# Kernel optimization log

Hardware: AMD Instinct MI355X
Metric: run time of the kernel (lower is better)

Reference implementation:

```python
import jax, jax.numpy as jnp
import numpy as np

B, NPG, KMAX, DIN, DOUT = 64, 2048, 64, 256, 256
HEADS, HDIM, EDIM = 2, 8, 16


def _ln(x, g, b, eps=1e-5):
    m = x.mean(-1, keepdims=True)
    v = x.var(-1, keepdims=True)
    return (x - m) / jnp.sqrt(v + eps) * g + b


def _lin_init(key, fan_in, fan_out):
    # xavier_uniform with gain=0.5 as in _init_weights
    lim = 0.5 * np.sqrt(6.0 / (fan_in + fan_out))
    return jax.random.uniform(key, (fan_in, fan_out), jnp.float32, -lim, lim)


def setup_inputs() -> dict:
    key = jax.random.key(0)
    ks = jax.random.split(key, 16)
    N = B * NPG
    inp = {
        "x": jax.random.normal(ks[0], (N, DIN), jnp.float32),
        # roughly orthonormal-scale eigenvector columns
        "eigenvectors": jax.random.normal(ks[1], (N, KMAX), jnp.float32) / np.sqrt(NPG),
        "eigenvalues": jax.random.uniform(ks[2], (B * KMAX,), jnp.float32, 0.0, 2.0),
        "eig_mask": jnp.ones((B * KMAX,), bool),
        "batch": jnp.repeat(jnp.arange(B, dtype=jnp.int32), NPG),
        "bsz": B,
        # eig_encoder: Linear(1,16), LayerNorm(16), ReLU, Linear(16,16)
        "W1": _lin_init(ks[3], 1, EDIM), "b1": jnp.zeros(EDIM),
        "g1": jnp.ones(EDIM), "be1": jnp.zeros(EDIM),
        "W2": _lin_init(ks[4], EDIM, EDIM), "b2": jnp.zeros(EDIM),
        # MultiheadAttention(16, 2 heads)
        "Wq": _lin_init(ks[5], EDIM, EDIM), "bq": jnp.zeros(EDIM),
        "Wk": _lin_init(ks[6], EDIM, EDIM), "bk": jnp.zeros(EDIM),
        "Wv": _lin_init(ks[7], EDIM, EDIM), "bv": jnp.zeros(EDIM),
        "Wo": _lin_init(ks[8], EDIM, EDIM), "bo": jnp.zeros(EDIM),
        # filter_generator: Linear(16,32), ReLU, Linear(32,1), Tanh
        "Wf1": _lin_init(ks[9], EDIM, 32), "bf1": jnp.zeros(32),
        "Wf2": _lin_init(ks[10], 32, 1), "bf2": jnp.zeros(1),
        # output_proj: Linear(in_dim,out_dim), LayerNorm(out_dim)
        "Wp": _lin_init(ks[11], DIN, DOUT), "bp": jnp.zeros(DOUT),
        "gp": jnp.ones(DOUT), "bep": jnp.zeros(DOUT),
    }
    return inp


def reference(x, eigenvectors, eigenvalues, eig_mask, batch, bsz,
              W1, b1, g1, be1, W2, b2,
              Wq, bq, Wk, bk, Wv, bv, Wo, bo,
              Wf1, bf1, Wf2, bf2, Wp, bp, gp, bep):
    N, D = x.shape
    k_max = eigenvalues.shape[0] // bsz
    ev = eigenvalues.reshape(bsz, k_max)            # [B, k]
    m = eig_mask.reshape(bsz, k_max)                # [B, k] valid mask

    # eig_encoder
    h = jnp.maximum(_ln(ev[..., None] @ W1 + b1, g1, be1), 0.0) @ W2 + b2  # [B, k, 16]

    # multi-head self-attention over eigenvalue tokens (eval mode, no dropout)
    q = (h @ Wq + bq).reshape(bsz, k_max, HEADS, HDIM)
    kk = (h @ Wk + bk).reshape(bsz, k_max, HEADS, HDIM)
    v = (h @ Wv + bv).reshape(bsz, k_max, HEADS, HDIM)
    scores = jnp.einsum('bqhd,bkhd->bhqk', q, kk) / np.sqrt(HDIM)
    scores = jnp.where(m[:, None, None, :], scores, -1e9)  # key_padding_mask
    attn = jax.nn.softmax(scores, axis=-1)
    ctx = jnp.einsum('bhqk,bkhd->bqhd', attn, v).reshape(bsz, k_max, EDIM)
    ctx = ctx @ Wo + bo

    # per-eigenvalue scalar filters, zeroed at padded slots
    filt = jnp.tanh(jnp.maximum(ctx @ Wf1 + bf1, 0.0) @ Wf2 + bf2)[..., 0]  # [B, k]
    filt = filt * m

    # batched spectral filtering (equal-size graphs: N = bsz * npg)
    npg = N // bsz
    xg = x.reshape(bsz, npg, D)
    vg = eigenvectors.reshape(bsz, npg, k_max)
    x_freq = jnp.einsum('bnk,bnd->bkd', vg, xg)                # U^T x
    x_spatial = jnp.einsum('bnk,bkd->bnd', vg, filt[..., None] * x_freq)  # U diag(f) U^T x

    # output_proj: Linear + LayerNorm
    return _ln(x_spatial.reshape(N, D) @ Wp + bp, gp, bep)
```

## Files before the change

kernel.cpp:

```cpp
#include <hip/hip_runtime.h>
#include <math.h>

#define BATCH 64
#define NPG   2048
#define KMAX  64
#define DIN   256
#define DOUT  256
#define S_SPLIT 8

typedef __attribute__((ext_vector_type(4))) float f32x4;
typedef __attribute__((ext_vector_type(8))) short bf16x8;

__device__ __forceinline__ unsigned short f2b(float f) {
    unsigned int u = __float_as_uint(f);
    u = (u + 0x7fffu + ((u >> 16) & 1u)) >> 16;
    return (unsigned short)u;
}
__device__ __forceinline__ float b2f(unsigned short h) {
    return __uint_as_float(((unsigned int)h) << 16);
}
__device__ __forceinline__ unsigned int pk2(float a, float b) {
    return (unsigned int)f2b(a) | ((unsigned int)f2b(b) << 16);
}

__global__ __launch_bounds__(64) void k_filt(
    const float* __restrict__ ev,
    const float* __restrict__ W1, const float* __restrict__ b1,
    const float* __restrict__ g1, const float* __restrict__ be1,
    const float* __restrict__ W2, const float* __restrict__ b2,
    const float* __restrict__ Wq, const float* __restrict__ bq,
    const float* __restrict__ Wk, const float* __restrict__ bk,
    const float* __restrict__ Wv, const float* __restrict__ bv,
    const float* __restrict__ Wo, const float* __restrict__ bo,
    const float* __restrict__ Wf1, const float* __restrict__ bf1,
    const float* __restrict__ Wf2, const float* __restrict__ bf2,
    float* __restrict__ filt)
{
    int b = blockIdx.x;
    int t = threadIdx.x;
    __shared__ float kk_l[64][16];
    __shared__ float v_l[64][16];

    float e = ev[b * KMAX + t];

    float h0[16];
    float mean = 0.f;
    #pragma unroll
    for (int j = 0; j < 16; j++) { h0[j] = e * W1[j] + b1[j]; mean += h0[j]; }
    mean *= (1.f / 16.f);
    float var = 0.f;
    #pragma unroll
    for (int j = 0; j < 16; j++) { float d = h0[j] - mean; var += d * d; }
    var *= (1.f / 16.f);
    float rstd = rsqrtf(var + 1e-5f);
    #pragma unroll
    for (int j = 0; j < 16; j++)
        h0[j] = fmaxf((h0[j] - mean) * rstd * g1[j] + be1[j], 0.f);

    float h[16];
    #pragma unroll
    for (int j = 0; j < 16; j++) {
        float a = b2[j];
        #pragma unroll
        for (int i = 0; i < 16; i++) a += h0[i] * W2[i * 16 + j];
        h[j] = a;
    }

    float q[16];
    #pragma unroll
    for (int j = 0; j < 16; j++) {
        float aq = bq[j], ak = bk[j], av = bv[j];
        #pragma unroll
        for (int i = 0; i < 16; i++) {
            float hi = h[i];
            aq += hi * Wq[i * 16 + j];
            ak += hi * Wk[i * 16 + j];
            av += hi * Wv[i * 16 + j];
        }
        q[j] = aq; kk_l[t][j] = ak; v_l[t][j] = av;
    }
    __syncthreads();

    float ctx[16];
    const float scale = 0.35355339059327373f;
    #pragma unroll
    for (int hd = 0; hd < 2; hd++) {
        float mx = -1e30f;
        for (int u = 0; u < 64; u++) {
            float s = 0.f;
            #pragma unroll
            for (int d = 0; d < 8; d++) s += q[hd * 8 + d] * kk_l[u][hd * 8 + d];
            mx = fmaxf(mx, s * scale);
        }
        float den = 0.f;
        float c[8] = {0, 0, 0, 0, 0, 0, 0, 0};
        for (int u = 0; u < 64; u++) {
            float s = 0.f;
            #pragma unroll
            for (int d = 0; d < 8; d++) s += q[hd * 8 + d] * kk_l[u][hd * 8 + d];
            float p = expf(s * scale - mx);
            den += p;
            #pragma unroll
            for (int d = 0; d < 8; d++) c[d] += p * v_l[u][hd * 8 + d];
        }
        float r = 1.f / den;
        #pragma unroll
        for (int d = 0; d < 8; d++) ctx[hd * 8 + d] = c[d] * r;
    }

    float c2[16];
    #pragma unroll
    for (int j = 0; j < 16; j++) {
        float a = bo[j];
        #pragma unroll
        for (int i = 0; i < 16; i++) a += ctx[i] * Wo[i * 16 + j];
        c2[j] = a;
    }

    float acc = bf2[0];
    #pragma unroll
    for (int j = 0; j < 32; j++) {
        float a = bf1[j];
        #pragma unroll
        for (int i = 0; i < 16; i++) a += c2[i] * Wf1[i * 32 + j];
        acc += fmaxf(a, 0.f) * Wf2[j];
    }
    filt[b * KMAX + t] = tanhf(acc);
}

__global__ __launch_bounds__(256) void k_xfreq(
    const float* __restrict__ x,
    const float* __restrict__ evec,
    unsigned short* __restrict__ part)
{
    int b = blockIdx.x;
    int s = blockIdx.y;
    int tid = threadIdx.x;
    int kg = tid >> 5;
    int dg = tid & 31;
    const int NS = NPG / S_SPLIT;
    int n0 = s * NS;

    __shared__ float xl[16][DIN];
    __shared__ float vl[16][KMAX];

    float acc[8][8];
    #pragma unroll
    for (int i = 0; i < 8; i++)
        #pragma unroll
        for (int j = 0; j < 8; j++) acc[i][j] = 0.f;

    for (int c = 0; c < NS; c += 16) {
        const float4* xsrc = (const float4*)(x + (size_t)(b * NPG + n0 + c) * DIN);
        const float4* vsrc = (const float4*)(evec + (size_t)(b * NPG + n0 + c) * KMAX);
        #pragma unroll
        for (int r = 0; r < 4; r++)
            ((float4*)xl)[r * 256 + tid] = xsrc[r * 256 + tid];
        ((float4*)vl)[tid] = vsrc[tid];
        __syncthreads();

        #pragma unroll 4
        for (int i = 0; i < 16; i++) {
            float4 va = *(const float4*)&vl[i][kg * 8];
            float4 vb = *(const float4*)&vl[i][kg * 8 + 4];
            float vk[8] = {va.x, va.y, va.z, va.w, vb.x, vb.y, vb.z, vb.w};
            float xd[8];
            #pragma unroll
            for (int j = 0; j < 8; j++) xd[j] = xl[i][dg + j * 32];
            #pragma unroll
            for (int kk = 0; kk < 8; kk++)
                #pragma unroll
                for (int j = 0; j < 8; j++)
                    acc[kk][j] += vk[kk] * xd[j];
        }
        __syncthreads();
    }

    unsigned short* dst = part + ((size_t)s * BATCH + b) * KMAX * DIN;
    #pragma unroll
    for (int kk = 0; kk < 8; kk++) {
        int k = kg * 8 + kk;
        #pragma unroll
        for (int j = 0; j < 8; j++)
            dst[k * DIN + dg + j * 32] = f2b(acc[kk][j]);
    }
}

__global__ __launch_bounds__(256) void k_gspec(
    const unsigned short* __restrict__ part, const float* __restrict__ filt,
    const float* __restrict__ Wp, unsigned short* __restrict__ g_frag)
{
    int b = blockIdx.x;
    int sg = blockIdx.y;
    int s = sg >> 2, g = sg & 3;
    int d = threadIdx.x;

    __shared__ float fxl[8][257];

    #pragma unroll
    for (int j = 0; j < 8; j++) {
        int k = 32 * s + 8 * g + j;
        float a = 0.f;
        #pragma unroll
        for (int ss = 0; ss < S_SPLIT; ss++)
            a += b2f(part[((size_t)(ss * BATCH + b) * KMAX + k) * DIN + d]);
        fxl[j][d] = a * filt[b * KMAX + k];
    }
    __syncthreads();

    float a[8] = {0.f, 0.f, 0.f, 0.f, 0.f, 0.f, 0.f, 0.f};
    #pragma unroll 4
    for (int dd = 0; dd < 256; dd++) {
        float w = Wp[(size_t)dd * DOUT + d];
        #pragma unroll
        for (int j = 0; j < 8; j++) a[j] += fxl[j][dd] * w;
    }

    int t = d >> 4, c = d & 15;
    uint4 p;
    p.x = pk2(a[0], a[1]); p.y = pk2(a[2], a[3]);
    p.z = pk2(a[4], a[5]); p.w = pk2(a[6], a[7]);
    *(uint4*)&g_frag[(((size_t)(b * 2 + s) * 16 + t) * 64 + (g * 16 + c)) * 8] = p;
}

#define VG_P 72

__global__ __launch_bounds__(256) void k_out(
    const float* __restrict__ evec,
    const unsigned short* __restrict__ g_frag,
    const float* __restrict__ bp, const float* __restrict__ gp,
    const float* __restrict__ bep,
    float* __restrict__ out)
{
    int blk = blockIdx.x;
    int b = blk >> 5;
    int n0 = blk * 64;
    int tid = threadIdx.x;
    int w = tid >> 6;
    int lane = tid & 63;
    int c = lane & 15, g = lane >> 4;

    __shared__ unsigned short lds_vg[64 * VG_P];

    {
        const float4* src = (const float4*)(evec + (size_t)n0 * KMAX);
        #pragma unroll
        for (int r = 0; r < 4; r++) {
            int f = r * 256 + tid;
            float4 v = src[f];
            int n = f >> 4, kq = f & 15;
            uint2 p; p.x = pk2(v.x, v.y); p.y = pk2(v.z, v.w);
            *(uint2*)&lds_vg[n * VG_P + kq * 4] = p;
        }
    }
    __syncthreads();

    f32x4 acc[16];
    #pragma unroll
    for (int t = 0; t < 16; t++) acc[t] = (f32x4){0.f, 0.f, 0.f, 0.f};

    bf16x8 a0 = *(const bf16x8*)&lds_vg[(16 * w + c) * VG_P + 8 * g];
    bf16x8 a1 = *(const bf16x8*)&lds_vg[(16 * w + c) * VG_P + 32 + 8 * g];

    const bf16x8* gf = (const bf16x8*)(g_frag + (size_t)b * 2 * 16 * 64 * 8);
    #pragma unroll
    for (int t = 0; t < 16; t++) {
        bf16x8 bb = gf[t * 64 + lane];
        acc[t] = __builtin_amdgcn_mfma_f32_16x16x32_bf16(a0, bb, acc[t], 0, 0, 0);
    }
    #pragma unroll
    for (int t = 0; t < 16; t++) {
        bf16x8 bb = gf[(16 + t) * 64 + lane];
        acc[t] = __builtin_amdgcn_mfma_f32_16x16x32_bf16(a1, bb, acc[t], 0, 0, 0);
    }

    #pragma unroll
    for (int r = 0; r < 4; r++) {
        float s1 = 0.f, s2 = 0.f;
        #pragma unroll
        for (int t = 0; t < 16; t++) {
            float a = acc[t][r] + bp[16 * t + c];
            s1 += a; s2 += a * a;
        }
        #pragma unroll
        for (int off = 1; off < 16; off <<= 1) {
            s1 += __shfl_xor(s1, off, 64);
            s2 += __shfl_xor(s2, off, 64);
        }
        float mean = s1 * (1.f / DOUT);
        float rstd = rsqrtf(s2 * (1.f / DOUT) - mean * mean + 1e-5f);
        int row = n0 + 16 * w + 4 * g + r;
        #pragma unroll
        for (int t = 0; t < 16; t++) {
            float a = acc[t][r] + bp[16 * t + c];
            out[(size_t)row * DOUT + 16 * t + c] =
                (a - mean) * rstd * gp[16 * t + c] + bep[16 * t + c];
        }
    }
}

extern "C" void kernel_launch(void* const* d_in, const int* in_sizes, int n_in,
                              void* d_out, int out_size, void* d_ws, size_t ws_size,
                              hipStream_t stream) {
    const float* x    = (const float*)d_in[0];
    const float* evec = (const float*)d_in[1];
    const float* ev   = (const float*)d_in[2];
    const float* W1  = (const float*)d_in[6];
    const float* b1  = (const float*)d_in[7];
    const float* g1  = (const float*)d_in[8];
    const float* be1 = (const float*)d_in[9];
    const float* W2  = (const float*)d_in[10];
    const float* b2  = (const float*)d_in[11];
    const float* Wq  = (const float*)d_in[12];
    const float* bq  = (const float*)d_in[13];
    const float* Wk  = (const float*)d_in[14];
    const float* bk  = (const float*)d_in[15];
    const float* Wv  = (const float*)d_in[16];
    const float* bv  = (const float*)d_in[17];
    const float* Wo  = (const float*)d_in[18];
    const float* bo  = (const float*)d_in[19];
    const float* Wf1 = (const float*)d_in[20];
    const float* bf1 = (const float*)d_in[21];
    const float* Wf2 = (const float*)d_in[22];
    const float* bf2 = (const float*)d_in[23];
    const float* Wp  = (const float*)d_in[24];
    const float* bp  = (const float*)d_in[25];
    const float* gp  = (const float*)d_in[26];
    const float* bep = (const float*)d_in[27];

    unsigned short* part   = (unsigned short*)d_ws;
    unsigned short* g_frag = part + (size_t)S_SPLIT * BATCH * KMAX * DIN;
    float*          filt   = (float*)(g_frag + (size_t)BATCH * KMAX * DIN);
    float* out = (float*)d_out;

    k_filt<<<BATCH, 64, 0, stream>>>(ev, W1, b1, g1, be1, W2, b2,
                                     Wq, bq, Wk, bk, Wv, bv, Wo, bo,
                                     Wf1, bf1, Wf2, bf2, filt);
    k_xfreq<<<dim3(BATCH, S_SPLIT), 256, 0, stream>>>(x, evec, part);
    k_gspec<<<dim3(BATCH, 8), 256, 0, stream>>>(part, filt, Wp, g_frag);
    k_out<<<(BATCH * NPG) / 64, 256, 0, stream>>>(evec, g_frag,
                                                  bp, gp, bep, out);
}
```

Measured before the change: 490.1 us.

## Compute U^T x projection with bf16 MFMA instead of FP32 FMA loops

Rewrites the k_xfreq kernel so x and eigenvector tiles are loaded, converted to bf16, and packed into MFMA fragment layout in shared memory, then accumulated with 16x16x32 bf16 matrix-core instructions. The block grows to 512 threads, 8 waves, each owning a 16-row k tile and half of the d columns. This targets the scalar FMA cost of the old register-tiled loop, which likely dominated the biggest stage. It gives up input precision to bf16, and the global loads are strided, with each lane reading eight rows of one column.

Measured after the change: 464.5 us. 1.06x faster.

```diff
diff --git a/kernel.cpp b/kernel.cpp
--- a/kernel.cpp
+++ b/kernel.cpp
@@ -128,7 +128,7 @@
     filt[b * KMAX + t] = tanhf(acc);
 }
 
-__global__ __launch_bounds__(256) void k_xfreq(
+__global__ __launch_bounds__(512) void k_xfreq(
     const float* __restrict__ x,
     const float* __restrict__ evec,
     unsigned short* __restrict__ part)
@@ -136,53 +136,73 @@
     int b = blockIdx.x;
     int s = blockIdx.y;
     int tid = threadIdx.x;
-    int kg = tid >> 5;
-    int dg = tid & 31;
+    int w = tid >> 6;
+    int lane = tid & 63;
+    int c = lane & 15, g = lane >> 4;
     const int NS = NPG / S_SPLIT;
-    int n0 = s * NS;
-
-    __shared__ float xl[16][DIN];
-    __shared__ float vl[16][KMAX];
-
-    float acc[8][8];
-    #pragma unroll
-    for (int i = 0; i < 8; i++)
-        #pragma unroll
-        for (int j = 0; j < 8; j++) acc[i][j] = 0.f;
-
-    for (int c = 0; c < NS; c += 16) {
-        const float4* xsrc = (const float4*)(x + (size_t)(b * NPG + n0 + c) * DIN);
-        const float4* vsrc = (const float4*)(evec + (size_t)(b * NPG + n0 + c) * KMAX);
-        #pragma unroll
-        for (int r = 0; r < 4; r++)
-            ((float4*)xl)[r * 256 + tid] = xsrc[r * 256 + tid];
-        ((float4*)vl)[tid] = vsrc[tid];
+    int n0 = b * NPG + s * NS;
+
+    __shared__ unsigned short xB[2 * 16 * 64 * 8];
+    __shared__ unsigned short evA[2 * 4 * 64 * 8];
+
+    f32x4 acc[8];
+    #pragma unroll
+    for (int t = 0; t < 8; t++) acc[t] = (f32x4){0.f, 0.f, 0.f, 0.f};
+
+    int mt = w & 3;
+    int dh = w >> 2;
+
+    for (int ch = 0; ch < NS; ch += 64) {
+        #pragma unroll
+        for (int i = 0; i < 4; i++) {
+            int idx = w * 4 + i;
+            int s2 = idx >> 4, t = idx & 15;
+            const float* src = x + (size_t)(n0 + ch + 32 * s2 + 8 * g) * DIN
+                                 + 16 * t + c;
+            float v[8];
+            #pragma unroll
+            for (int j = 0; j < 8; j++) v[j] = src[(size_t)j * DIN];
+            uint4 p;
+            p.x = pk2(v[0], v[1]); p.y = pk2(v[2], v[3]);
+            p.z = pk2(v[4], v[5]); p.w = pk2(v[6], v[7]);
+            *(uint4*)&xB[((size_t)idx * 64 + lane) * 8] = p;
+        }
+        {
+            int s2 = w >> 2, kt = w & 3;
+            const float* src = evec + (size_t)(n0 + ch + 32 * s2 + 8 * g) * KMAX
+                                    + 16 * kt + c;
+            float v[8];
+            #pragma unroll
+            for (int j = 0; j < 8; j++) v[j] = src[(size_t)j * KMAX];
+            uint4 p;
+            p.x = pk2(v[0], v[1]); p.y = pk2(v[2], v[3]);
+            p.z = pk2(v[4], v[5]); p.w = pk2(v[6], v[7]);
+            *(uint4*)&evA[((size_t)w * 64 + lane) * 8] = p;
+        }
         __syncthreads();
 
-        #pragma unroll 4
-        for (int i = 0; i < 16; i++) {
-            float4 va = *(const float4*)&vl[i][kg * 8];
-            float4 vb = *(const float4*)&vl[i][kg * 8 + 4];
-            float vk[8] = {va.x, va.y, va.z, va.w, vb.x, vb.y, vb.z, vb.w};
-            float xd[8];
-            #pragma unroll
-            for (int j = 0; j < 8; j++) xd[j] = xl[i][dg + j * 32];
-            #pragma unroll
-            for (int kk = 0; kk < 8; kk++)
-                #pragma unroll
-                for (int j = 0; j < 8; j++)
-                    acc[kk][j] += vk[kk] * xd[j];
+        #pragma unroll
+        for (int s2 = 0; s2 < 2; s2++) {
+            bf16x8 a = *(const bf16x8*)&evA[((s2 * 4 + mt) * 64 + lane) * 8];
+            #pragma unroll
+            for (int tt = 0; tt < 8; tt++) {
+                int t = 8 * dh + tt;
+                bf16x8 bb = *(const bf16x8*)&xB[((s2 * 16 + t) * 64 + lane) * 8];
+                acc[tt] = __builtin_amdgcn_mfma_f32_16x16x32_bf16(a, bb, acc[tt], 0, 0, 0);
+            }
         }
         __syncthreads();
     }
 
-    unsigned short* dst = part + ((size_t)s * BATCH + b) * KMAX * DIN;
-    #pragma unroll
-    for (int kk = 0; kk < 8; kk++) {
-        int k = kg * 8 + kk;
-        #pragma unroll
-        for (int j = 0; j < 8; j++)
-            dst[k * DIN + dg + j * 32] = f2b(acc[kk][j]);
+    unsigned short* dst = part + (size_t)(s * BATCH + b) * KMAX * DIN;
+    #pragma unroll
+    for (int tt = 0; tt < 8; tt++) {
+        int d = 16 * (8 * dh + tt) + c;
+        #pragma unroll
+        for (int r = 0; r < 4; r++) {
+            int k = 16 * mt + 4 * g + r;
+            dst[(size_t)k * DIN + d] = f2b(acc[tt][r]);
+        }
     }
 }
 
@@ -336,7 +356,7 @@
     k_filt<<<BATCH, 64, 0, stream>>>(ev, W1, b1, g1, be1, W2, b2,
                                      Wq, bq, Wk, bk, Wv, bv, Wo, bo,
                                      Wf1, bf1, Wf2, bf2, filt);
-    k_xfreq<<<dim3(BATCH, S_SPLIT), 256, 0, stream>>>(x, evec, part);
+    k_xfreq<<<dim3(BATCH, S_SPLIT), 512, 0, stream>>>(x, evec, part);
     k_gspec<<<dim3(BATCH, 8), 256, 0, stream>>>(part, filt, Wp, g_frag);
     k_out<<<(BATCH * NPG) / 64, 256, 0, stream>>>(evec, g_frag,
                                                   bp, gp, bep, out);
```
